# Optimization experiments

Hardware: AMD Instinct MI355X
Metric: run time of the kernel (lower is better)

The kernel has to match this reference:

```python
import jax, jax.numpy as jnp
import numpy as np

B, N_COL, D, CAT_SIZE = 8192, 32, 512, 10
N_PAIR = N_COL // 2  # columns alternate: even=numerical(tanh,size1), odd=categorical(logsoftmax,size10)


def setup_inputs() -> dict:
    key = jax.random.key(0)
    ks = jax.random.split(key, 3)
    s = 1.0 / np.sqrt(D).astype(np.float32)
    return {
        "x": jax.random.normal(ks[0], (B, N_COL, D), jnp.float32),
        "W_num": jax.random.normal(ks[1], (N_PAIR, D, 1), jnp.float32) * s,
        "b_num": jnp.zeros((N_PAIR, 1), jnp.float32),
        "W_cat": jax.random.normal(ks[2], (N_PAIR, D, CAT_SIZE), jnp.float32) * s,
        "b_cat": jnp.zeros((N_PAIR, CAT_SIZE), jnp.float32),
    }


def reference(x, W_num, b_num, W_cat, b_cat):
    # Even columns: Linear(D->1) + Tanh  (numerical). Batched over the 16 columns.
    x_num = x[:, 0::2, :]                                            # [B, 16, D]
    out_num = jnp.tanh(jnp.einsum('bnd,ndo->bno', x_num, W_num) + b_num)[..., 0]  # [B, 16]

    # Odd columns: Linear(D->10) + LogSoftmax, then argmax over categories.
    x_cat = x[:, 1::2, :]                                            # [B, 16, D]
    logits = jnp.einsum('bnd,ndo->bno', x_cat, W_cat) + b_cat        # [B, 16, 10]
    logp = jax.nn.log_softmax(logits, axis=-1)
    out_cat = jnp.argmax(logp, axis=-1).astype(x.dtype)              # [B, 16]

    # Re-interleave columns back to original order 0..31 and concat on last dim.
    return jnp.stack([out_num, out_cat], axis=-1).reshape(x.shape[0], N_COL)  # [B, 32]
```

## Files before the change

kernel.cpp:

```cpp
#include <hip/hip_runtime.h>
#include <math.h>

#define NCOL 32
#define DDIM 512
#define NPAIR 16
#define CATS 10
#define ROW_STRIDE (NCOL * DDIM)
#define NBODY 192
#define TOTROWS 8192

template <int CTRL, int ROW_MASK>
__device__ __forceinline__ float dpp_add(float v) {
    int t = __builtin_amdgcn_update_dpp(0, __float_as_int(v), CTRL, ROW_MASK, 0xf, false);
    return v + __int_as_float(t);
}
template <int CTRL, int ROW_MASK>
__device__ __forceinline__ float dpp_mov(float v) {
    int t = __builtin_amdgcn_update_dpp(0, __float_as_int(v), CTRL, ROW_MASK, 0xf, false);
    return __int_as_float(t);
}

__device__ __forceinline__ float wave_reduce_halves(float v) {
    v = dpp_add<0x111, 0xf>(v);
    v = dpp_add<0x112, 0xf>(v);
    v = dpp_add<0x114, 0xf>(v);
    v = dpp_add<0x118, 0xf>(v);
    v = dpp_add<0x142, 0xa>(v);
    return v;
}
__device__ __forceinline__ float wave_reduce_full(float v) {
    v = wave_reduce_halves(v);
    v = dpp_add<0x143, 0xc>(v);
    return v;
}

#define WAITVM(n)  asm volatile("s_waitcnt vmcnt(" #n ")" ::: "memory")
#define WAITLGKM() asm volatile("s_waitcnt lgkmcnt(0)" ::: "memory")

#define ISSUE(row, slot) do {                                                  \
    const float* _g = x + (size_t)(row) * ROW_STRIDE + xcoloff;                \
    float* _l = &slab[wslot][slot][0];                                         \
    _Pragma("unroll")                                                          \
    for (int _k = 0; _k < 4; ++_k)                                             \
        __builtin_amdgcn_global_load_lds(                                      \
            (const __attribute__((address_space(1))) unsigned int*)            \
                (_g + _k * 256 + lane * 4),                                    \
            (__attribute__((address_space(3))) unsigned int*)(_l + _k * 256),  \
            16, 0, 0);                                                         \
} while (0)

#define STEP(WAITSTMT, ISSUESTMT) do {                                         \
    WAITSTMT;                                                                  \
    const float* pb = &slab[wslot][s][0];                                      \
    float4 Ea = *(const float4*)(pb +   0 + 4 * lane);                         \
    float4 Eb = *(const float4*)(pb + 256 + 4 * lane);                         \
    float4 Oa = *(const float4*)(pb + 512 + 4 * lane);                         \
    float4 Ob = *(const float4*)(pb + 768 + 4 * lane);                         \
    WAITLGKM();                                                                \
    ISSUESTMT;                                                                 \
    double best = -1.0e300;                                                    \
    int bi = 0;                                                                \
    _Pragma("unroll")                                                          \
    for (int c = 0; c < CATS; ++c) {                                           \
        float sc = Oa.x * wc[c];                                               \
        sc = fmaf(Oa.y, wc[10 + c], sc);                                       \
        sc = fmaf(Oa.z, wc[20 + c], sc);                                       \
        sc = fmaf(Oa.w, wc[30 + c], sc);                                       \
        sc = fmaf(Ob.x, wc[40 + c], sc);                                       \
        sc = fmaf(Ob.y, wc[50 + c], sc);                                       \
        sc = fmaf(Ob.z, wc[60 + c], sc);                                       \
        sc = fmaf(Ob.w, wc[70 + c], sc);                                       \
        sc = wave_reduce_halves(sc);                                           \
        float slo = dpp_mov<0x143, 0xc>(sc);                                   \
        double d = (double)sc + (double)slo + biasd[c];                        \
        if (d > best) { best = d; bi = c; }                                    \
    }                                                                          \
    float sn = Ea.x * w[0];                                                    \
    sn = fmaf(Ea.y, w[1], sn);                                                 \
    sn = fmaf(Ea.z, w[2], sn);                                                 \
    sn = fmaf(Ea.w, w[3], sn);                                                 \
    sn = fmaf(Eb.x, w[4], sn);                                                 \
    sn = fmaf(Eb.y, w[5], sn);                                                 \
    sn = fmaf(Eb.z, w[6], sn);                                                 \
    sn = fmaf(Eb.w, w[7], sn);                                                 \
    sn = wave_reduce_full(sn);                                                 \
    if (lane == 63) {                                                          \
        float2 o2 = make_float2(tanhf(sn + bias), (float)bi);                  \
        *(float2*)(out + (size_t)r * NCOL + 2 * p) = o2;                       \
    }                                                                          \
    s = (s == 2) ? 0 : s + 1;                                                  \
    r += NBODY;                                                                \
} while (0)

__global__ __launch_bounds__(256, 3) void pair_sweep_kernel(
    const float* __restrict__ x,
    const float* __restrict__ Wn,
    const float* __restrict__ bn,
    const float* __restrict__ Wc,
    const float* __restrict__ bc,
    float* __restrict__ out)
{
    __shared__ __align__(16) float slab[4][3][1024];

    const int lane  = threadIdx.x & 63;
    const int wslot = threadIdx.x >> 6;
    const int q     = __builtin_amdgcn_readfirstlane(blockIdx.x & 3);
    const int body  = __builtin_amdgcn_readfirstlane(blockIdx.x >> 2);
    const int p     = __builtin_amdgcn_readfirstlane(q * 4 + wslot);
    const size_t xcoloff = (size_t)p * (2 * DDIM);

    float w[8];
    {
        float4 wa = *(const float4*)(Wn + p * DDIM + lane * 4);
        float4 wb = *(const float4*)(Wn + p * DDIM + 256 + lane * 4);
        w[0]=wa.x; w[1]=wa.y; w[2]=wa.z; w[3]=wa.w;
        w[4]=wb.x; w[5]=wb.y; w[6]=wb.z; w[7]=wb.w;
    }
    const float bias = __int_as_float(
        __builtin_amdgcn_readfirstlane(__float_as_int(bn[p])));

    float wc[80];
    {
        const float* w0 = Wc + ((size_t)p * DDIM + lane * 4) * CATS;
        const float* w1 = Wc + ((size_t)p * DDIM + 256 + lane * 4) * CATS;
        #pragma unroll
        for (int k = 0; k < 10; ++k) {
            float4 t = *(const float4*)(w0 + k * 4);
            wc[4*k] = t.x; wc[4*k+1] = t.y; wc[4*k+2] = t.z; wc[4*k+3] = t.w;
        }
        #pragma unroll
        for (int k = 0; k < 10; ++k) {
            float4 t = *(const float4*)(w1 + k * 4);
            wc[40+4*k] = t.x; wc[40+4*k+1] = t.y; wc[40+4*k+2] = t.z; wc[40+4*k+3] = t.w;
        }
    }
    double biasd[CATS];
    #pragma unroll
    for (int c = 0; c < CATS; ++c)
        biasd[c] = (double)__int_as_float(
            __builtin_amdgcn_readfirstlane(__float_as_int(bc[p * CATS + c])));

    const int n = __builtin_amdgcn_readfirstlane(
        (TOTROWS - body + NBODY - 1) / NBODY);

    ISSUE(body,             0);
    ISSUE(body + NBODY,     1);
    ISSUE(body + 2 * NBODY, 2);

    int s = 0;
    int r = body;
    int ri = body + 3 * NBODY;
    for (int j = 0; j < n - 3; ++j) {
        STEP(WAITVM(8), { ISSUE(ri, s); ri += NBODY; });
    }
    STEP(WAITVM(8), {});
    STEP(WAITVM(5), {});
    STEP(WAITVM(1), {});
}

extern "C" void kernel_launch(void* const* d_in, const int* in_sizes, int n_in,
                              void* d_out, int out_size, void* d_ws, size_t ws_size,
                              hipStream_t stream) {
    const float* x  = (const float*)d_in[0];
    const float* Wn = (const float*)d_in[1];
    const float* bn = (const float*)d_in[2];
    const float* Wc = (const float*)d_in[3];
    const float* bc = (const float*)d_in[4];
    float* out = (float*)d_out;

    hipLaunchKernelGGL(pair_sweep_kernel, dim3(768), dim3(256), 0, stream,
                       x, Wn, bn, Wc, bc, out);
}
```

Measured before the change: 102.5 us.

## Software-pipeline LDS fragment reads one row ahead of compute

Restructures the per-row loop so the LDS-to-register fragment read for the next row is issued before computing the current row, using double-buffered register fragments (A/B). The explicit lgkmcnt(0) wait goes away, so LDS read latency can overlap the FMA and DPP reduction work. The slot rotation and vmcnt thresholds are reworked with a longer prologue and epilogue. In exchange it uses 16 more VGPRs under a 3-wave occupancy bound, and it relies on the compiler inserting correct lgkm waits plus hand-tuned vmcnt counts being right.

```diff
diff --git a/kernel.cpp b/kernel.cpp
--- a/kernel.cpp
+++ b/kernel.cpp
@@ -35,7 +35,6 @@
 }
 
 #define WAITVM(n)  asm volatile("s_waitcnt vmcnt(" #n ")" ::: "memory")
-#define WAITLGKM() asm volatile("s_waitcnt lgkmcnt(0)" ::: "memory")
 
 #define ISSUE(row, slot) do {                                                  \
     const float* _g = x + (size_t)(row) * ROW_STRIDE + xcoloff;                \
@@ -49,50 +48,51 @@
             16, 0, 0);                                                         \
 } while (0)
 
-#define STEP(WAITSTMT, ISSUESTMT) do {                                         \
-    WAITSTMT;                                                                  \
-    const float* pb = &slab[wslot][s][0];                                      \
-    float4 Ea = *(const float4*)(pb +   0 + 4 * lane);                         \
-    float4 Eb = *(const float4*)(pb + 256 + 4 * lane);                         \
-    float4 Oa = *(const float4*)(pb + 512 + 4 * lane);                         \
-    float4 Ob = *(const float4*)(pb + 768 + 4 * lane);                         \
-    WAITLGKM();                                                                \
-    ISSUESTMT;                                                                 \
+#define FRAGREAD(slot) do {                                                    \
+    const float* _pb = &slab[wslot][slot][0];                                  \
+    B0 = *(const float4*)(_pb +   0 + 4 * lane);                               \
+    B1 = *(const float4*)(_pb + 256 + 4 * lane);                               \
+    B2 = *(const float4*)(_pb + 512 + 4 * lane);                               \
+    B3 = *(const float4*)(_pb + 768 + 4 * lane);                               \
+} while (0)
+
+#define COMPUTE(row) do {                                                      \
     double best = -1.0e300;                                                    \
     int bi = 0;                                                                \
     _Pragma("unroll")                                                          \
     for (int c = 0; c < CATS; ++c) {                                           \
-        float sc = Oa.x * wc[c];                                               \
-        sc = fmaf(Oa.y, wc[10 + c], sc);                                       \
-        sc = fmaf(Oa.z, wc[20 + c], sc);                                       \
-        sc = fmaf(Oa.w, wc[30 + c], sc);                                       \
-        sc = fmaf(Ob.x, wc[40 + c], sc);                                       \
-        sc = fmaf(Ob.y, wc[50 + c], sc);                                       \
-        sc = fmaf(Ob.z, wc[60 + c], sc);                                       \
-        sc = fmaf(Ob.w, wc[70 + c], sc);                                       \
+        float sc = A2.x * wc[c];                                               \
+        sc = fmaf(A2.y, wc[10 + c], sc);                                       \
+        sc = fmaf(A2.z, wc[20 + c], sc);                                       \
+        sc = fmaf(A2.w, wc[30 + c], sc);                                       \
+        sc = fmaf(A3.x, wc[40 + c], sc);                                       \
+        sc = fmaf(A3.y, wc[50 + c], sc);                                       \
+        sc = fmaf(A3.z, wc[60 + c], sc);                                       \
+        sc = fmaf(A3.w, wc[70 + c], sc);                                       \
         sc = wave_reduce_halves(sc);                                           \
         float slo = dpp_mov<0x143, 0xc>(sc);                                   \
         double d = (double)sc + (double)slo + biasd[c];                        \
         if (d > best) { best = d; bi = c; }                                    \
     }                                                                          \
-    float sn = Ea.x * w[0];                                                    \
-    sn = fmaf(Ea.y, w[1], sn);                                                 \
-    sn = fmaf(Ea.z, w[2], sn);                                                 \
-    sn = fmaf(Ea.w, w[3], sn);                                                 \
-    sn = fmaf(Eb.x, w[4], sn);                                                 \
-    sn = fmaf(Eb.y, w[5], sn);                                                 \
-    sn = fmaf(Eb.z, w[6], sn);                                                 \
-    sn = fmaf(Eb.w, w[7], sn);                                                 \
+    float sn = A0.x * w[0];                                                    \
+    sn = fmaf(A0.y, w[1], sn);                                                 \
+    sn = fmaf(A0.z, w[2], sn);                                                 \
+    sn = fmaf(A0.w, w[3], sn);                                                 \
+    sn = fmaf(A1.x, w[4], sn);                                                 \
+    sn = fmaf(A1.y, w[5], sn);                                                 \
+    sn = fmaf(A1.z, w[6], sn);                                                 \
+    sn = fmaf(A1.w, w[7], sn);                                                 \
     sn = wave_reduce_full(sn);                                                 \
     if (lane == 63) {                                                          \
         float2 o2 = make_float2(tanhf(sn + bias), (float)bi);                  \
-        *(float2*)(out + (size_t)r * NCOL + 2 * p) = o2;                       \
+        *(float2*)(out + (size_t)(row) * NCOL + 2 * p) = o2;                   \
     }                                                                          \
-    s = (s == 2) ? 0 : s + 1;                                                  \
-    r += NBODY;                                                                \
 } while (0)
 
-__global__ __launch_bounds__(256, 3) void pair_sweep_kernel(
+#define SWAPAB() do { A0 = B0; A1 = B1; A2 = B2; A3 = B3; } while (0)
+#define WRAP3(v) do { v = (v == 2) ? 0 : v + 1; } while (0)
+
+__global__ __launch_bounds__(256, 3) void pair_pipe_kernel(
     const float* __restrict__ x,
     const float* __restrict__ Wn,
     const float* __restrict__ bn,
@@ -143,19 +143,56 @@
     const int n = __builtin_amdgcn_readfirstlane(
         (TOTROWS - body + NBODY - 1) / NBODY);
 
+    float4 A0, A1, A2, A3, B0, B1, B2, B3;
+
     ISSUE(body,             0);
     ISSUE(body + NBODY,     1);
     ISSUE(body + 2 * NBODY, 2);
-
-    int s = 0;
-    int r = body;
+    WAITVM(8);
+    {
+        const float* _pb = &slab[wslot][0][0];
+        A0 = *(const float4*)(_pb +   0 + 4 * lane);
+        A1 = *(const float4*)(_pb + 256 + 4 * lane);
+        A2 = *(const float4*)(_pb + 512 + 4 * lane);
+        A3 = *(const float4*)(_pb + 768 + 4 * lane);
+    }
+
+    int r  = body;
     int ri = body + 3 * NBODY;
-    for (int j = 0; j < n - 3; ++j) {
-        STEP(WAITVM(8), { ISSUE(ri, s); ri += NBODY; });
-    }
-    STEP(WAITVM(8), {});
-    STEP(WAITVM(5), {});
-    STEP(WAITVM(1), {});
+    int si = 0;
+    int sr = 1;
+
+    ISSUE(ri, si); ri += NBODY;
+    WAITVM(8);
+    FRAGREAD(sr);
+    COMPUTE(r); r += NBODY;
+    SWAPAB(); WRAP3(si); WRAP3(sr);
+
+    ISSUE(ri, si); ri += NBODY;
+    WAITVM(9);
+    FRAGREAD(sr);
+    COMPUTE(r); r += NBODY;
+    SWAPAB(); WRAP3(si); WRAP3(sr);
+
+    for (int j = 2; j <= n - 4; ++j) {
+        ISSUE(ri, si); ri += NBODY;
+        WAITVM(10);
+        FRAGREAD(sr);
+        COMPUTE(r); r += NBODY;
+        SWAPAB(); WRAP3(si); WRAP3(sr);
+    }
+
+    WAITVM(6);
+    FRAGREAD(sr);
+    COMPUTE(r); r += NBODY;
+    SWAPAB(); WRAP3(sr);
+
+    WAITVM(2);
+    FRAGREAD(sr);
+    COMPUTE(r); r += NBODY;
+    SWAPAB();
+
+    COMPUTE(r);
 }
 
 extern "C" void kernel_launch(void* const* d_in, const int* in_sizes, int n_in,
@@ -168,6 +205,6 @@
     const float* bc = (const float*)d_in[4];
     float* out = (float*)d_out;
 
-    hipLaunchKernelGGL(pair_sweep_kernel, dim3(768), dim3(256), 0, stream,
+    hipLaunchKernelGGL(pair_pipe_kernel, dim3(768), dim3(256), 0, stream,
                        x, Wn, bn, Wc, bc, out);
 }
```

Result: slower. 108.7 us (+6.0%).
